# Kernel optimization log

Measured on AMD Instinct MI355X. Metric: run time of the kernel, lower is better.

## Reference

```python
import jax, jax.numpy as jnp
import numpy as np

B, N, F_IN, T, K, F_OUT = 16, 1024, 64, 12, 3, 64


def setup_inputs() -> dict:
    key = jax.random.key(0)
    ks = jax.random.split(key, 8)
    s = 0.05  # keep sigmoid/softmax in a sane range
    return {
        "x": jax.random.normal(ks[0], (B, N, F_IN, T), dtype=jnp.float32),
        "W1": jax.random.normal(ks[1], (T,), dtype=jnp.float32) * s,
        "W2": jax.random.normal(ks[2], (F_IN, T), dtype=jnp.float32) * s,
        "W3": jax.random.normal(ks[3], (F_IN,), dtype=jnp.float32) * s,
        "bs": jax.random.normal(ks[4], (1, N, N), dtype=jnp.float32) * s,
        "Vs": jax.random.normal(ks[5], (N, N), dtype=jnp.float32) * s,
        "cheb": jax.random.normal(ks[6], (K, N, N), dtype=jnp.float32) * (1.0 / np.sqrt(N)),
        "Theta": jax.random.normal(ks[7], (K, F_IN, F_OUT), dtype=jnp.float32) * (1.0 / np.sqrt(F_IN)),
    }


def spatial_attention(x, W1, W2, W3, bs, Vs):
    # x: (B, N, F, T)
    lhs = jnp.einsum('bnft,t->bnf', x, W1) @ W2          # (B, N, T)
    rhs = jnp.einsum('f,bnft->bnt', W3, x)               # (B, N, T); torch transpose folded into einsum below
    product = jnp.einsum('bnt,bmt->bnm', lhs, rhs)       # (B, N, N)
    S = jnp.einsum('nm,bmk->bnk', Vs, jax.nn.sigmoid(product + bs))
    return jax.nn.softmax(S, axis=1)                     # softmax over dim=1 as in torch


def reference(x, W1, W2, W3, bs, Vs, cheb, Theta):
    # Spatial attention gate (B, N, N)
    S = spatial_attention(x, W1, W2, W3, bs, Vs)
    # K-order Chebyshev graph conv, vectorized over all T timesteps at once.
    # Loop over K (small, structurally distinct Theta_k) keeps peak memory low.
    out = jnp.zeros((B, N, F_OUT, T), dtype=x.dtype)
    for k in range(K):
        T_k_at = cheb[k][None, :, :] * S                 # (B, N, N) attention-weighted polynomial
        # torch: T_k_at.permute(0,2,1) @ graph_signal  ->  contract over source-node dim m
        rhs = jnp.einsum('bmn,bmft->bnft', T_k_at, x)    # (B, N, F_in, T)
        out = out + jnp.einsum('bnft,fo->bnot', rhs, Theta[k])
    return jax.nn.relu(out)                              # (B, N, F_out, T)
```

## Files before the change

kernel.cpp:

```cpp
#include <hip/hip_runtime.h>


typedef __attribute__((ext_vector_type(8))) short v8s;
typedef __attribute__((ext_vector_type(4))) float v4f;
typedef unsigned short u16;
typedef unsigned int u32;

#define Bn 16
#define Nn 1024
#define Tn 12
#define CT 768
#define KK 3072

__device__ inline u16 f2bf(float f) {
  u32 u = __float_as_uint(f);
  return (u16)((u + 0x8000u) >> 16);
}
__device__ inline float bf2f(u16 h) { return __uint_as_float(((u32)h) << 16); }

__device__ inline void gl_lds16(const void* g, void* l) {
  __builtin_amdgcn_global_load_lds(
      (const __attribute__((address_space(1))) u32*)g,
      (__attribute__((address_space(3))) u32*)l, 16, 0, 0);
}

__global__ __launch_bounds__(256) void k_attn_lr(
    const float* __restrict__ x, const float* __restrict__ W1,
    const float* __restrict__ W2, const float* __restrict__ W3,
    float* __restrict__ lhs, float* __restrict__ rhs)
{
  int bn   = blockIdx.x * 4 + (threadIdx.x >> 6);
  int lane = threadIdx.x & 63;
  const float* xp = x + (size_t)bn * (64 * Tn) + lane * Tn;
  float4 v0 = *(const float4*)(xp);
  float4 v1 = *(const float4*)(xp + 4);
  float4 v2 = *(const float4*)(xp + 8);
  float xv[12] = {v0.x, v0.y, v0.z, v0.w, v1.x, v1.y, v1.z, v1.w,
                  v2.x, v2.y, v2.z, v2.w};
  float w3 = W3[lane];
  float tmp = 0.f;
#pragma unroll
  for (int t = 0; t < 12; ++t) tmp += xv[t] * W1[t];
#pragma unroll
  for (int t = 0; t < 12; ++t) {
    float v = tmp * W2[lane * 12 + t];
    float r = w3 * xv[t];
#pragma unroll
    for (int off = 32; off; off >>= 1) {
      v += __shfl_xor(v, off);
      r += __shfl_xor(r, off);
    }
    if (lane == t) {
      lhs[(size_t)bn * 12 + t] = v;
      rhs[(size_t)bn * 12 + t] = r;
    }
  }
}

__global__ __launch_bounds__(256) void k_vs16(const float* __restrict__ Vs,
                                              u16* __restrict__ V16)
{
  size_t i = (size_t)blockIdx.x * 256 + threadIdx.x;
  float4 v = *(const float4*)(Vs + i * 4);
  *(ushort4*)(V16 + i * 4) =
      make_ushort4(f2bf(v.x), f2bf(v.y), f2bf(v.z), f2bf(v.w));
}

__global__ __launch_bounds__(256) void k_xtf(const float* __restrict__ x,
                                             u16* __restrict__ xTf)
{
  __shared__ u16 xs[32][768];
  int b = blockIdx.y, m0 = blockIdx.x * 32;
  const float* xb = x + ((size_t)b * Nn + m0) * CT;
  int tid = threadIdx.x;
#pragma unroll
  for (int q = 0; q < 24; ++q) {
    int idx = (q * 256 + tid) * 4;
    int i = idx / 768, j = idx % 768;
    float4 v = *(const float4*)(xb + (size_t)i * CT + j);
    xs[i][j]     = f2bf(v.x);
    xs[i][j + 1] = f2bf(v.y);
    xs[i][j + 2] = f2bf(v.z);
    xs[i][j + 3] = f2bf(v.w);
  }
  __syncthreads();
#pragma unroll
  for (int q = 0; q < 24; ++q) {
    int flat = q * 256 + tid;
    int t = flat >> 9;
    int rem = flat & 511;
    int i = rem >> 4, fq = rem & 15;
    ushort4 o;
    o.x = xs[i][(fq * 4 + 0) * 12 + t];
    o.y = xs[i][(fq * 4 + 1) * 12 + t];
    o.z = xs[i][(fq * 4 + 2) * 12 + t];
    o.w = xs[i][(fq * 4 + 3) * 12 + t];
    *(ushort4*)(xTf + (((size_t)b * 12 + t) * Nn + m0 + i) * 64 + fq * 4) = o;
  }
}

__global__ __launch_bounds__(256) void k_prod(
    const float* __restrict__ lhs, const float* __restrict__ rhs,
    const float* __restrict__ bs, u16* __restrict__ Pt)
{
  __shared__ float ls[1024][13];
  __shared__ float rs[16][12];
  int b = blockIdx.y, c0 = blockIdx.x * 16;
  int tid = threadIdx.x;
  const float* lb = lhs + (size_t)b * Nn * 12;
#pragma unroll
  for (int mq = 0; mq < 4; ++mq) {
    int m = mq * 256 + tid;
    const float* p = lb + (size_t)m * 12;
    float4 a0 = *(const float4*)p;
    float4 a1 = *(const float4*)(p + 4);
    float4 a2 = *(const float4*)(p + 8);
    ls[m][0] = a0.x; ls[m][1] = a0.y; ls[m][2]  = a0.z; ls[m][3]  = a0.w;
    ls[m][4] = a1.x; ls[m][5] = a1.y; ls[m][6]  = a1.z; ls[m][7]  = a1.w;
    ls[m][8] = a2.x; ls[m][9] = a2.y; ls[m][10] = a2.z; ls[m][11] = a2.w;
  }
  if (tid < 192) {
    int cc = tid / 12, tt = tid % 12;
    rs[cc][tt] = rhs[((size_t)b * Nn + c0 + cc) * 12 + tt];
  }
  __syncthreads();
  u16* Pb = Pt + ((size_t)b << 20);
#pragma unroll
  for (int mq = 0; mq < 4; ++mq) {
    int m = mq * 256 + tid;
    float l[12];
#pragma unroll
    for (int t = 0; t < 12; ++t) l[t] = ls[m][t];
#pragma unroll
    for (int cc = 0; cc < 16; ++cc) {
      float d = bs[(size_t)m * Nn + c0 + cc];
#pragma unroll
      for (int t = 0; t < 12; ++t) d += l[t] * rs[cc][t];
      float sg = 1.f / (1.f + __expf(-d));
      Pb[(size_t)(c0 + cc) * Nn + m] = f2bf(sg);
    }
  }
}

__global__ __launch_bounds__(512, 2) void k_gemm_vsP8(
    const u16* __restrict__ A, const u16* __restrict__ Pt,
    float* __restrict__ Spre)
{
  extern __shared__ u16 smem[];
  u16* AsL = smem;
  u16* BsL = smem + 32768;
  const int tid = threadIdx.x;
  const int lane = tid & 63;
  const int w = tid >> 6;
  const int wr = w >> 2, wc = w & 3;
  const int l15 = lane & 15, h = lane >> 4;

  const int bi = blockIdx.x;
  const int L = (bi & 7) * 32 + (bi >> 3);
  const int b = L >> 4;
  const int rem = L & 15;
  const int n0 = (rem >> 2) * 256;
  const int c0 = (rem & 3) * 256;
  const u16* Ag = A;
  const u16* Bg = Pt + ((size_t)b << 20);

  int aro[4], bro[4], akc[4], dst[4];
#pragma unroll
  for (int i = 0; i < 4; ++i) {
    int ch = i * 512 + tid;
    int row = ch >> 3;
    int kc = (ch & 7) ^ (row & 7);
    aro[i] = n0 + row; bro[i] = c0 + row; akc[i] = kc;
    dst[i] = ch * 8;
  }

#define STAGE_V(t, buf) do {                                              \
    const u16* As_ = Ag + (size_t)(t) * 64;                               \
    const u16* Bs_ = Bg + (size_t)(t) * 64;                               \
    _Pragma("unroll")                                                     \
    for (int i_ = 0; i_ < 4; ++i_) {                                      \
      gl_lds16(As_ + (size_t)aro[i_] * Nn + akc[i_] * 8,                  \
               AsL + (buf) * 16384 + dst[i_]);                            \
      gl_lds16(Bs_ + (size_t)bro[i_] * Nn + akc[i_] * 8,                  \
               BsL + (buf) * 16384 + dst[i_]);                            \
    } } while (0)

  v4f acc[8][4] = {};
  STAGE_V(0, 0);
  STAGE_V(1, 1);

  const int NT = Nn / 64;
  for (int t = 0; t < NT; ++t) {
    const int cur = t & 1;
    if (t < NT - 1) asm volatile("s_waitcnt vmcnt(8)" ::: "memory");
    else            asm volatile("s_waitcnt vmcnt(0)" ::: "memory");
    __builtin_amdgcn_s_barrier();
    const u16* Ab = AsL + cur * 16384;
    const u16* Bb = BsL + cur * 16384;
#pragma unroll
    for (int ks = 0; ks < 2; ++ks) {
      v8s a[8], bf[4];
#pragma unroll
      for (int mi = 0; mi < 8; ++mi) {
        int rA = wr * 128 + mi * 16 + l15;
        a[mi] = *(const v8s*)(Ab + rA * 64 + (((ks * 4 + h) ^ (rA & 7)) * 8));
      }
#pragma unroll
      for (int nj = 0; nj < 4; ++nj) {
        int rB = wc * 64 + nj * 16 + l15;
        bf[nj] = *(const v8s*)(Bb + rB * 64 + (((ks * 4 + h) ^ (rB & 7)) * 8));
      }
      __builtin_amdgcn_s_setprio(1);
#pragma unroll
      for (int mi = 0; mi < 8; ++mi)
#pragma unroll
        for (int nj = 0; nj < 4; ++nj)
          acc[mi][nj] = __builtin_amdgcn_mfma_f32_16x16x32_bf16(
              a[mi], bf[nj], acc[mi][nj], 0, 0, 0);
      __builtin_amdgcn_s_setprio(0);
    }
    asm volatile("s_waitcnt lgkmcnt(0)" ::: "memory");
    __builtin_amdgcn_s_barrier();
    if (t + 2 < NT) STAGE_V(t + 2, cur);
  }
#undef STAGE_V

  float* Sp = Spre + ((size_t)b << 20);
#pragma unroll
  for (int mi = 0; mi < 8; ++mi) {
    int rown = n0 + wr * 128 + mi * 16 + h * 4;
#pragma unroll
    for (int nj = 0; nj < 4; ++nj) {
      int colc = c0 + wc * 64 + nj * 16 + l15;
      *(float4*)(Sp + (size_t)colc * Nn + rown) = *(float4*)&acc[mi][nj];
    }
  }
}

__global__ __launch_bounds__(256) void k_soft(const float* __restrict__ Spre,
                                              u16* __restrict__ St)
{
  int wid = threadIdx.x >> 6, lane = threadIdx.x & 63;
  int row = blockIdx.x * 4 + wid;
  int b = blockIdx.y;
  const float* p = Spre + ((size_t)b << 20) + (size_t)row * Nn;
  float v[16];
#pragma unroll
  for (int q = 0; q < 4; ++q) {
    float4 t = *(const float4*)(p + q * 256 + lane * 4);
    v[q * 4 + 0] = t.x; v[q * 4 + 1] = t.y;
    v[q * 4 + 2] = t.z; v[q * 4 + 3] = t.w;
  }
  float M = v[0];
#pragma unroll
  for (int i = 1; i < 16; ++i) M = fmaxf(M, v[i]);
#pragma unroll
  for (int off = 32; off; off >>= 1) M = fmaxf(M, __shfl_xor(M, off));
  float s = 0.f;
#pragma unroll
  for (int i = 0; i < 16; ++i) { v[i] = __expf(v[i] - M); s += v[i]; }
#pragma unroll
  for (int off = 32; off; off >>= 1) s += __shfl_xor(s, off);
  float inv = 1.f / s;
  u16* o = St + ((size_t)b << 20) + (size_t)row * Nn;
#pragma unroll
  for (int q = 0; q < 4; ++q) {
    u32 w0 = (u32)f2bf(v[q * 4 + 0] * inv) | ((u32)f2bf(v[q * 4 + 1] * inv) << 16);
    u32 w1 = (u32)f2bf(v[q * 4 + 2] * inv) | ((u32)f2bf(v[q * 4 + 3] * inv) << 16);
    *(uint2*)(o + q * 256 + lane * 4) = make_uint2(w0, w1);
  }
}

__global__ __launch_bounds__(256) void k_tht(const float* __restrict__ Theta,
                                             u16* __restrict__ ThT)
{
  int tid = threadIdx.x;
#pragma unroll
  for (int q = 0; q < 48; ++q) {
    int flat = q * 256 + tid;
    int ko = flat >> 6, f = flat & 63;
    int k = ko >> 6, o = ko & 63;
    ThT[flat] = f2bf(Theta[((size_t)k * 64 + f) * 64 + o]);
  }
}

__global__ __launch_bounds__(256) void k_as3(const float* __restrict__ cheb,
                                             const u16* __restrict__ St,
                                             u16* __restrict__ AS)
{
  __shared__ float ch[3][64][65];
  int b = blockIdx.z, m0 = blockIdx.y * 64, n0 = blockIdx.x * 64;
  int tid = threadIdx.x;
#pragma unroll
  for (int kk = 0; kk < 3; ++kk)
#pragma unroll
    for (int q = 0; q < 16; ++q) {
      int idx = q * 256 + tid;
      int i = idx >> 6, j = idx & 63;
      ch[kk][i][j] =
          cheb[((size_t)kk << 20) + (size_t)(m0 + i) * Nn + n0 + j];
    }
  __syncthreads();
  const u16* Stb = St + ((size_t)b << 20);
#pragma unroll
  for (int q = 0; q < 16; ++q) {
    int idx = q * 256 + tid;
    int i = idx >> 6, j = idx & 63;
    float s = bf2f(Stb[(size_t)(n0 + i) * Nn + m0 + j]);
    size_t base = ((size_t)b * Nn + n0 + i) * KK + m0 + j;
#pragma unroll
    for (int kk = 0; kk < 3; ++kk)
      AS[base + (size_t)kk * Nn] = f2bf(ch[kk][j][i] * s);
  }
}

__global__ __launch_bounds__(256) void k_thx3(const u16* __restrict__ xTf,
                                              const u16* __restrict__ ThT,
                                              u16* __restrict__ TX)
{
  int b = blockIdx.z, t = blockIdx.y;
  int mh = blockIdx.x & 1, kk = blockIdx.x >> 1;
  int lane = threadIdx.x & 63, w = threadIdx.x >> 6;
  int l15 = lane & 15, h = lane >> 4;
  int mbase = mh * 512 + w * 128;
  const u16* xb = xTf + ((size_t)b * 12 + t) * Nn * 64;
  const u16* Tk = ThT + (size_t)kk * 4096;
  u16* ob = TX + ((size_t)b * CT + t) * KK + (size_t)kk * Nn;

  v8s bfr[4][2];
#pragma unroll
  for (int nj = 0; nj < 4; ++nj)
#pragma unroll
    for (int q = 0; q < 2; ++q)
      bfr[nj][q] = *(const v8s*)(Tk + (nj * 16 + l15) * 64 + (q * 4 + h) * 8);

#pragma unroll
  for (int mi = 0; mi < 8; ++mi) {
    int m = mbase + mi * 16;
    v8s a0 = *(const v8s*)(xb + (size_t)(m + l15) * 64 + h * 8);
    v8s a1 = *(const v8s*)(xb + (size_t)(m + l15) * 64 + 32 + h * 8);
#pragma unroll
    for (int nj = 0; nj < 4; ++nj) {
      v4f acc = {};
      acc = __builtin_amdgcn_mfma_f32_16x16x32_bf16(a0, bfr[nj][0], acc, 0, 0, 0);
      acc = __builtin_amdgcn_mfma_f32_16x16x32_bf16(a1, bfr[nj][1], acc, 0, 0, 0);
      int o = nj * 16 + l15;
      ushort4 st = make_ushort4(f2bf(acc[0]), f2bf(acc[1]), f2bf(acc[2]),
                                f2bf(acc[3]));
      *(ushort4*)(ob + (size_t)o * (12 * KK) + m + h * 4) = st;
    }
  }
}

__global__ __launch_bounds__(512, 2) void k_gemm_out8(
    const u16* __restrict__ AS, const u16* __restrict__ TX,
    float* __restrict__ out)
{
  extern __shared__ u16 smem[];
  u16* AsL = smem;
  u16* BsL = smem + 32768;
  const int tid = threadIdx.x;
  const int lane = tid & 63;
  const int w = tid >> 6;
  const int wr = w >> 2, wc = w & 3;
  const int l15 = lane & 15, h = lane >> 4;

  const int bi = blockIdx.x;
  const int L = (bi & 7) * 32 + (bi >> 3);
  const int b = L >> 4;
  const int rem = L & 15;
  const int n0 = (rem >> 2) * 256;
  const int c0 = (rem & 3) * 192;
  const u16* Ag = AS + (size_t)b * Nn * KK;
  const u16* Bg = TX + (size_t)b * CT * KK;

  int aro[4], akc[4], adst[4];
#pragma unroll
  for (int i = 0; i < 4; ++i) {
    int ch = i * 512 + tid;
    int row = ch >> 3;
    akc[i] = (ch & 7) ^ (row & 7);
    aro[i] = n0 + row;
    adst[i] = ch * 8;
  }
  int bro[3], bkc[3], bdst[3];
#pragma unroll
  for (int i = 0; i < 3; ++i) {
    int ch = i * 512 + tid;
    int row = ch >> 3;
    bkc[i] = (ch & 7) ^ (row & 7);
    bro[i] = c0 + row;
    bdst[i] = ch * 8;
  }

#define STAGE_O(t, buf) do {                                              \
    const u16* As_ = Ag + (size_t)(t) * 64;                               \
    const u16* Bs_ = Bg + (size_t)(t) * 64;                               \
    _Pragma("unroll")                                                     \
    for (int i_ = 0; i_ < 4; ++i_)                                        \
      gl_lds16(As_ + (size_t)aro[i_] * KK + akc[i_] * 8,                  \
               AsL + (buf) * 16384 + adst[i_]);                           \
    _Pragma("unroll")                                                     \
    for (int i_ = 0; i_ < 3; ++i_)                                        \
      gl_lds16(Bs_ + (size_t)bro[i_] * KK + bkc[i_] * 8,                  \
               BsL + (buf) * 12288 + bdst[i_]);                           \
    } while (0)

  v4f acc[8][3] = {};
  STAGE_O(0, 0);
  STAGE_O(1, 1);

  const int NT = KK / 64;
  for (int t = 0; t < NT; ++t) {
    const int cur = t & 1;
    if (t < NT - 1) asm volatile("s_waitcnt vmcnt(7)" ::: "memory");
    else            asm volatile("s_waitcnt vmcnt(0)" ::: "memory");
    __builtin_amdgcn_s_barrier();
    const u16* Ab = AsL + cur * 16384;
    const u16* Bb = BsL + cur * 12288;
#pragma unroll
    for (int ks = 0; ks < 2; ++ks) {
      v8s a[8], bf[3];
#pragma unroll
      for (int mi = 0; mi < 8; ++mi) {
        int rA = wr * 128 + mi * 16 + l15;
        a[mi] = *(const v8s*)(Ab + rA * 64 + (((ks * 4 + h) ^ (rA & 7)) * 8));
      }
#pragma unroll
      for (int nj = 0; nj < 3; ++nj) {
        int rB = wc * 48 + nj * 16 + l15;
        bf[nj] = *(const v8s*)(Bb + rB * 64 + (((ks * 4 + h) ^ (rB & 7)) * 8));
      }
      __builtin_amdgcn_s_setprio(1);
#pragma unroll
      for (int mi = 0; mi < 8; ++mi)
#pragma unroll
        for (int nj = 0; nj < 3; ++nj)
          acc[mi][nj] = __builtin_amdgcn_mfma_f32_16x16x32_bf16(
              a[mi], bf[nj], acc[mi][nj], 0, 0, 0);
      __builtin_amdgcn_s_setprio(0);
    }
    asm volatile("s_waitcnt lgkmcnt(0)" ::: "memory");
    __builtin_amdgcn_s_barrier();
    if (t + 2 < NT) STAGE_O(t + 2, cur);
  }
#undef STAGE_O

  float* ob = out + (size_t)b * Nn * CT;
#pragma unroll
  for (int mi = 0; mi < 8; ++mi) {
    int rown = n0 + wr * 128 + mi * 16 + h * 4;
#pragma unroll
    for (int nj = 0; nj < 3; ++nj) {
      int colc = c0 + wc * 48 + nj * 16 + l15;
#pragma unroll
      for (int r = 0; r < 4; ++r)
        ob[(size_t)(rown + r) * CT + colc] = fmaxf(acc[mi][nj][r], 0.f);
    }
  }
}

extern "C" void kernel_launch(void* const* d_in, const int* in_sizes, int n_in,
                              void* d_out, int out_size, void* d_ws,
                              size_t ws_size, hipStream_t stream)
{
  const float* x     = (const float*)d_in[0];
  const float* W1    = (const float*)d_in[1];
  const float* W2    = (const float*)d_in[2];
  const float* W3    = (const float*)d_in[3];
  const float* bs    = (const float*)d_in[4];
  const float* Vs    = (const float*)d_in[5];
  const float* cheb  = (const float*)d_in[6];
  const float* Theta = (const float*)d_in[7];
  float* out = (float*)d_out;

  const size_t BNT = (size_t)Bn * Nn * Tn;
  char* w = (char*)d_ws;
  float* lhs  = (float*)w;                        w += BNT * 4;
  float* rhs  = (float*)w;                        w += BNT * 4;
  u16*   AS   = (u16*)w;
  u16*   Pt   = AS;
  float* Spre = (float*)(w + ((size_t)32 << 20));
  w += (size_t)96 << 20;
  u16*   St   = (u16*)w;                          w += (size_t)32 << 20;
  u16*   xTf  = (u16*)w;                          w += (size_t)Bn * 12 * Nn * 64 * 2;
  u16*   TX   = (u16*)w;                          w += (size_t)Bn * CT * KK * 2;
  u16*   Vs16 = (u16*)w;                          w += (size_t)Nn * Nn * 2;
  u16*   ThT  = (u16*)w;

  (void)hipFuncSetAttribute((const void*)k_gemm_vsP8,
                            hipFuncAttributeMaxDynamicSharedMemorySize, 131072);
  (void)hipFuncSetAttribute((const void*)k_gemm_out8,
                            hipFuncAttributeMaxDynamicSharedMemorySize, 114688);

  k_attn_lr<<<(Bn * Nn) / 4, 256, 0, stream>>>(x, W1, W2, W3, lhs, rhs);
  k_vs16<<<1024, 256, 0, stream>>>(Vs, Vs16);
  k_xtf<<<dim3(Nn / 32, Bn), 256, 0, stream>>>(x, xTf);
  k_prod<<<dim3(Nn / 16, Bn), 256, 0, stream>>>(lhs, rhs, bs, Pt);
  k_gemm_vsP8<<<256, 512, 131072, stream>>>(Vs16, Pt, Spre);
  k_soft<<<dim3(Nn / 4, Bn), 256, 0, stream>>>(Spre, St);
  k_tht<<<1, 256, 0, stream>>>(Theta, ThT);
  k_thx3<<<dim3(6, 12, Bn), 256, 0, stream>>>(xTf, ThT, TX);
  k_as3<<<dim3(Nn / 64, Nn / 64, Bn), 256, 0, stream>>>(cheb, St, AS);
  k_gemm_out8<<<256, 512, 114688, stream>>>(AS, TX, out);
}
```

Before: 418.3 us.

## Fuse softmax with cheb-weighted AS build and fold xTf into attention kernel

Result: faster. 376.6 us (-10.0%).

```diff
diff --git a/kernel.cpp b/kernel.cpp
--- a/kernel.cpp
+++ b/kernel.cpp
@@ -27,7 +27,7 @@
 __global__ __launch_bounds__(256) void k_attn_lr(
     const float* __restrict__ x, const float* __restrict__ W1,
     const float* __restrict__ W2, const float* __restrict__ W3,
-    float* __restrict__ lhs, float* __restrict__ rhs)
+    float* __restrict__ lhs, float* __restrict__ rhs, u16* __restrict__ xTf)
 {
   int bn   = blockIdx.x * 4 + (threadIdx.x >> 6);
   int lane = threadIdx.x & 63;
@@ -37,6 +37,11 @@
   float4 v2 = *(const float4*)(xp + 8);
   float xv[12] = {v0.x, v0.y, v0.z, v0.w, v1.x, v1.y, v1.z, v1.w,
                   v2.x, v2.y, v2.z, v2.w};
+  int b = bn >> 10, m = bn & 1023;
+#pragma unroll
+  for (int t = 0; t < 12; ++t)
+    xTf[(((size_t)b * 12 + t) * Nn + m) * 64 + lane] = f2bf(xv[t]);
+
   float w3 = W3[lane];
   float tmp = 0.f;
 #pragma unroll
@@ -66,36 +71,26 @@
       make_ushort4(f2bf(v.x), f2bf(v.y), f2bf(v.z), f2bf(v.w));
 }
 
-__global__ __launch_bounds__(256) void k_xtf(const float* __restrict__ x,
-                                             u16* __restrict__ xTf)
-{
-  __shared__ u16 xs[32][768];
-  int b = blockIdx.y, m0 = blockIdx.x * 32;
-  const float* xb = x + ((size_t)b * Nn + m0) * CT;
+__global__ __launch_bounds__(256) void k_chebT(const float* __restrict__ cheb,
+                                               float* __restrict__ chebT)
+{
+  __shared__ float tbuf[64][65];
+  int k = blockIdx.z, m0 = blockIdx.y * 64, n0 = blockIdx.x * 64;
+  const float* src = cheb + ((size_t)k << 20);
+  float* dst = chebT + ((size_t)k << 20);
   int tid = threadIdx.x;
 #pragma unroll
-  for (int q = 0; q < 24; ++q) {
-    int idx = (q * 256 + tid) * 4;
-    int i = idx / 768, j = idx % 768;
-    float4 v = *(const float4*)(xb + (size_t)i * CT + j);
-    xs[i][j]     = f2bf(v.x);
-    xs[i][j + 1] = f2bf(v.y);
-    xs[i][j + 2] = f2bf(v.z);
-    xs[i][j + 3] = f2bf(v.w);
+  for (int q = 0; q < 16; ++q) {
+    int idx = q * 256 + tid;
+    int i = idx >> 6, j = idx & 63;
+    tbuf[i][j] = src[(size_t)(m0 + i) * Nn + n0 + j];
   }
   __syncthreads();
 #pragma unroll
-  for (int q = 0; q < 24; ++q) {
-    int flat = q * 256 + tid;
-    int t = flat >> 9;
-    int rem = flat & 511;
-    int i = rem >> 4, fq = rem & 15;
-    ushort4 o;
-    o.x = xs[i][(fq * 4 + 0) * 12 + t];
-    o.y = xs[i][(fq * 4 + 1) * 12 + t];
-    o.z = xs[i][(fq * 4 + 2) * 12 + t];
-    o.w = xs[i][(fq * 4 + 3) * 12 + t];
-    *(ushort4*)(xTf + (((size_t)b * 12 + t) * Nn + m0 + i) * 64 + fq * 4) = o;
+  for (int q = 0; q < 16; ++q) {
+    int idx = q * 256 + tid;
+    int i = idx >> 6, j = idx & 63;
+    dst[(size_t)(n0 + i) * Nn + m0 + j] = tbuf[j][i];
   }
 }
 
@@ -237,8 +232,9 @@
   }
 }
 
-__global__ __launch_bounds__(256) void k_soft(const float* __restrict__ Spre,
-                                              u16* __restrict__ St)
+__global__ __launch_bounds__(256) void k_soft_as3(
+    const float* __restrict__ Spre, const float* __restrict__ chebT,
+    u16* __restrict__ AS)
 {
   int wid = threadIdx.x >> 6, lane = threadIdx.x & 63;
   int row = blockIdx.x * 4 + wid;
@@ -262,12 +258,20 @@
 #pragma unroll
   for (int off = 32; off; off >>= 1) s += __shfl_xor(s, off);
   float inv = 1.f / s;
-  u16* o = St + ((size_t)b << 20) + (size_t)row * Nn;
-#pragma unroll
-  for (int q = 0; q < 4; ++q) {
-    u32 w0 = (u32)f2bf(v[q * 4 + 0] * inv) | ((u32)f2bf(v[q * 4 + 1] * inv) << 16);
-    u32 w1 = (u32)f2bf(v[q * 4 + 2] * inv) | ((u32)f2bf(v[q * 4 + 3] * inv) << 16);
-    *(uint2*)(o + q * 256 + lane * 4) = make_uint2(w0, w1);
+  u16* o = AS + ((size_t)b * Nn + row) * KK;
+#pragma unroll
+  for (int kk = 0; kk < 3; ++kk) {
+    const float* ct = chebT + ((size_t)kk << 20) + (size_t)row * Nn;
+#pragma unroll
+    for (int q = 0; q < 4; ++q) {
+      int m = q * 256 + lane * 4;
+      float4 cv = *(const float4*)(ct + m);
+      ushort4 st = make_ushort4(f2bf(cv.x * v[q * 4 + 0] * inv),
+                                f2bf(cv.y * v[q * 4 + 1] * inv),
+                                f2bf(cv.z * v[q * 4 + 2] * inv),
+                                f2bf(cv.w * v[q * 4 + 3] * inv));
+      *(ushort4*)(o + kk * 1024 + m) = st;
+    }
   }
 }
 
@@ -281,36 +285,6 @@
     int ko = flat >> 6, f = flat & 63;
     int k = ko >> 6, o = ko & 63;
     ThT[flat] = f2bf(Theta[((size_t)k * 64 + f) * 64 + o]);
-  }
-}
-
-__global__ __launch_bounds__(256) void k_as3(const float* __restrict__ cheb,
-                                             const u16* __restrict__ St,
-                                             u16* __restrict__ AS)
-{
-  __shared__ float ch[3][64][65];
-  int b = blockIdx.z, m0 = blockIdx.y * 64, n0 = blockIdx.x * 64;
-  int tid = threadIdx.x;
-#pragma unroll
-  for (int kk = 0; kk < 3; ++kk)
-#pragma unroll
-    for (int q = 0; q < 16; ++q) {
-      int idx = q * 256 + tid;
-      int i = idx >> 6, j = idx & 63;
-      ch[kk][i][j] =
-          cheb[((size_t)kk << 20) + (size_t)(m0 + i) * Nn + n0 + j];
-    }
-  __syncthreads();
-  const u16* Stb = St + ((size_t)b << 20);
-#pragma unroll
-  for (int q = 0; q < 16; ++q) {
-    int idx = q * 256 + tid;
-    int i = idx >> 6, j = idx & 63;
-    float s = bf2f(Stb[(size_t)(n0 + i) * Nn + m0 + j]);
-    size_t base = ((size_t)b * Nn + n0 + i) * KK + m0 + j;
-#pragma unroll
-    for (int kk = 0; kk < 3; ++kk)
-      AS[base + (size_t)kk * Nn] = f2bf(ch[kk][j][i] * s);
   }
 }
 
@@ -418,31 +392,35 @@
     __builtin_amdgcn_s_barrier();
     const u16* Ab = AsL + cur * 16384;
     const u16* Bb = BsL + cur * 12288;
+    v8s a[2][8], bf[2][3];
 #pragma unroll
     for (int ks = 0; ks < 2; ++ks) {
-      v8s a[8], bf[3];
 #pragma unroll
       for (int mi = 0; mi < 8; ++mi) {
         int rA = wr * 128 + mi * 16 + l15;
-        a[mi] = *(const v8s*)(Ab + rA * 64 + (((ks * 4 + h) ^ (rA & 7)) * 8));
+        a[ks][mi] =
+            *(const v8s*)(Ab + rA * 64 + (((ks * 4 + h) ^ (rA & 7)) * 8));
       }
 #pragma unroll
       for (int nj = 0; nj < 3; ++nj) {
         int rB = wc * 48 + nj * 16 + l15;
-        bf[nj] = *(const v8s*)(Bb + rB * 64 + (((ks * 4 + h) ^ (rB & 7)) * 8));
+        bf[ks][nj] =
+            *(const v8s*)(Bb + rB * 64 + (((ks * 4 + h) ^ (rB & 7)) * 8));
       }
-      __builtin_amdgcn_s_setprio(1);
-#pragma unroll
-      for (int mi = 0; mi < 8; ++mi)
-#pragma unroll
-        for (int nj = 0; nj < 3; ++nj)
-          acc[mi][nj] = __builtin_amdgcn_mfma_f32_16x16x32_bf16(
-              a[mi], bf[nj], acc[mi][nj], 0, 0, 0);
-      __builtin_amdgcn_s_setprio(0);
     }
     asm volatile("s_waitcnt lgkmcnt(0)" ::: "memory");
     __builtin_amdgcn_s_barrier();
     if (t + 2 < NT) STAGE_O(t + 2, cur);
+    __builtin_amdgcn_s_setprio(1);
+#pragma unroll
+    for (int ks = 0; ks < 2; ++ks)
+#pragma unroll
+      for (int mi = 0; mi < 8; ++mi)
+#pragma unroll
+        for (int nj = 0; nj < 3; ++nj)
+          acc[mi][nj] = __builtin_amdgcn_mfma_f32_16x16x32_bf16(
+              a[ks][mi], bf[ks][nj], acc[mi][nj], 0, 0, 0);
+    __builtin_amdgcn_s_setprio(0);
   }
 #undef STAGE_O
 
@@ -474,33 +452,31 @@
   const float* Theta = (const float*)d_in[7];
   float* out = (float*)d_out;
 
-  const size_t BNT = (size_t)Bn * Nn * Tn;
-  char* w = (char*)d_ws;
-  float* lhs  = (float*)w;                        w += BNT * 4;
-  float* rhs  = (float*)w;                        w += BNT * 4;
-  u16*   AS   = (u16*)w;
-  u16*   Pt   = AS;
-  float* Spre = (float*)(w + ((size_t)32 << 20));
-  w += (size_t)96 << 20;
-  u16*   St   = (u16*)w;                          w += (size_t)32 << 20;
-  u16*   xTf  = (u16*)w;                          w += (size_t)Bn * 12 * Nn * 64 * 2;
-  u16*   TX   = (u16*)w;                          w += (size_t)Bn * CT * KK * 2;
-  u16*   Vs16 = (u16*)w;                          w += (size_t)Nn * Nn * 2;
-  u16*   ThT  = (u16*)w;
+  char* wsb = (char*)d_ws;
+  const size_t MB = (size_t)1 << 20;
+  float* lhs   = (float*)wsb;
+  float* rhs   = lhs + (size_t)Bn * Nn * Tn;
+  u16*   AS    = (u16*)(wsb + 2 * MB);
+  u16*   Pt    = AS;
+  float* Spre  = (float*)(wsb + 98 * MB);
+  u16*   TX    = (u16*)(wsb + 98 * MB);
+  float* chebT = (float*)(wsb + 170 * MB);
+  u16*   xTf   = (u16*)(wsb + 182 * MB);
+  u16*   Vs16  = (u16*)(wsb + 206 * MB);
+  u16*   ThT   = (u16*)(wsb + 208 * MB);
 
   (void)hipFuncSetAttribute((const void*)k_gemm_vsP8,
                             hipFuncAttributeMaxDynamicSharedMemorySize, 131072);
   (void)hipFuncSetAttribute((const void*)k_gemm_out8,
                             hipFuncAttributeMaxDynamicSharedMemorySize, 114688);
 
-  k_attn_lr<<<(Bn * Nn) / 4, 256, 0, stream>>>(x, W1, W2, W3, lhs, rhs);
+  k_attn_lr<<<(Bn * Nn) / 4, 256, 0, stream>>>(x, W1, W2, W3, lhs, rhs, xTf);
   k_vs16<<<1024, 256, 0, stream>>>(Vs, Vs16);
-  k_xtf<<<dim3(Nn / 32, Bn), 256, 0, stream>>>(x, xTf);
+  k_chebT<<<dim3(16, 16, 3), 256, 0, stream>>>(cheb, chebT);
   k_prod<<<dim3(Nn / 16, Bn), 256, 0, stream>>>(lhs, rhs, bs, Pt);
   k_gemm_vsP8<<<256, 512, 131072, stream>>>(Vs16, Pt, Spre);
-  k_soft<<<dim3(Nn / 4, Bn), 256, 0, stream>>>(Spre, St);
+  k_soft_as3<<<dim3(Nn / 4, Bn), 256, 0, stream>>>(Spre, chebT, AS);
   k_tht<<<1, 256, 0, stream>>>(Theta, ThT);
   k_thx3<<<dim3(6, 12, Bn), 256, 0, stream>>>(xTf, ThT, TX);
-  k_as3<<<dim3(Nn / 64, Nn / 64, Bn), 256, 0, stream>>>(cheb, St, AS);
   k_gemm_out8<<<256, 512, 114688, stream>>>(AS, TX, out);
 }
```
